# Performance work log

Hardware: AMD Instinct MI355X
Metric: run time of the kernel (lower is better)

Reference implementation:

```python
import jax, jax.numpy as jnp
import numpy as np

B, N, C = 32, 320, 768
H = 12
LT, LS = 64, 256
HD = C // H
MLP_H = 4 * C
EPS = 1e-5


def _ln(x, g, b):
    m = jnp.mean(x, axis=-1, keepdims=True)
    v = jnp.var(x, axis=-1, keepdims=True)
    return (x - m) * jax.lax.rsqrt(v + EPS) * g + b


def setup_inputs() -> dict:
    key = jax.random.key(0)
    ks = jax.random.split(key, 16)
    s = 0.02
    inp = {
        'x': jax.random.normal(ks[0], (B, N, C), jnp.float32),
        'global_index_template': jax.random.randint(ks[1], (B, LT), 0, LT),
        'global_index_search': jax.random.randint(ks[2], (B, LS), 0, LS),
        'g1': jnp.ones((C,), jnp.float32), 'b1': jnp.zeros((C,), jnp.float32),
        'Wqkv': jax.random.normal(ks[3], (C, 3 * C), jnp.float32) * s,
        'Wproj': jax.random.normal(ks[4], (C, C), jnp.float32) * s,
        'bproj': jnp.zeros((C,), jnp.float32),
        'g2': jnp.ones((C,), jnp.float32), 'b2': jnp.zeros((C,), jnp.float32),
        'W1': jax.random.normal(ks[5], (C, MLP_H), jnp.float32) * s,
        'bm1': jnp.zeros((MLP_H,), jnp.float32),
        'W2': jax.random.normal(ks[6], (MLP_H, C), jnp.float32) * s,
        'bm2': jnp.zeros((C,), jnp.float32),
        'Wg': jax.random.normal(ks[7], (C, C), jnp.float32) * s,
        'bg': jnp.zeros((C,), jnp.float32),
        'g3': jnp.ones((C,), jnp.float32), 'b3': jnp.zeros((C,), jnp.float32),
    }
    return inp


def reference(x, global_index_template, global_index_search, g1, b1, Wqkv, Wproj, bproj,
              g2, b2, W1, bm1, W2, bm2, Wg, bg, g3, b3):
    scale = HD ** (-0.5)
    # --- Attention ---
    xn = _ln(x, g1, b1)
    qkv = (xn @ Wqkv).reshape(B, N, 3, H, HD)
    q, k, v = qkv[:, :, 0], qkv[:, :, 1], qkv[:, :, 2]  # [B,N,H,HD]
    logits = jnp.einsum('bnhd,bmhd->bhnm', q, k) * scale
    attn = jax.nn.softmax(logits, axis=-1)  # [B,H,N,N]
    ctx = jnp.einsum('bhnm,bmhd->bnhd', attn, v).reshape(B, N, C)
    x = x + (ctx @ Wproj + bproj)
    # --- MLP ---
    h = jax.nn.gelu(_ln(x, g2, b2) @ W1 + bm1, approximate=False)
    x = x + (h @ W2 + bm2)
    # --- Block-adjacency from attention (avg pooling) ---
    w_ts = jnp.sum(attn[:, :, :LT, LT:], axis=1) / H  # [B,LT,LS]
    w_ts = jax.nn.softmax(w_ts, axis=2)
    adj = jnp.zeros((B, N, N), x.dtype)
    adj = adj.at[:, :LT, LT:].set(w_ts)
    adj = adj.at[:, LT:, :LT].set(jnp.swapaxes(w_ts, 1, 2))
    # --- GCN layer ---
    support = x @ Wg + bg
    x = jnp.einsum('bnm,bmc->bnc', adj, support)
    x = x + _ln(x, g3, b3)
    return x
```

## Files before the change

### kernel.cpp

```cpp
#include <hip/hip_runtime.h>
#include <stdint.h>

#define NB 32
#define NSEQ 320
#define CDIM 768
#define NH 12
#define HD 64
#define MLPH 3072
#define MROWS (NB*NSEQ)

typedef __attribute__((ext_vector_type(8))) short v8s;
typedef __attribute__((ext_vector_type(4))) float v4f;

__device__ __forceinline__ unsigned short f2b(float f){
  unsigned int u = __float_as_uint(f);
  u += 0x7fffu + ((u >> 16) & 1u);
  return (unsigned short)(u >> 16);
}
__device__ __forceinline__ float b2f(unsigned short h){
  return __uint_as_float(((unsigned int)h) << 16);
}
__device__ __forceinline__ void glds16(const unsigned short* g, unsigned short* l){
  __builtin_amdgcn_global_load_lds(
      (const __attribute__((address_space(1))) void*)g,
      (__attribute__((address_space(3))) void*)l, 16, 0, 0);
}

__global__ __launch_bounds__(256)
void castAll(const float* __restrict__ Wqkv, const float* __restrict__ Wproj,
             const float* __restrict__ W1,   const float* __restrict__ W2,
             const float* __restrict__ Wg,
             unsigned short* __restrict__ wqkvT, unsigned short* __restrict__ wprojT,
             unsigned short* __restrict__ w1T,   unsigned short* __restrict__ w2T,
             unsigned short* __restrict__ wgT){
  int bid = blockIdx.x;
  const float* W; unsigned short* Wt; int K, N, KT;
  if (bid < 1728){ W = Wqkv; Wt = wqkvT; K = 768; N = 2304; KT = 24; }
  else if (bid < 1728+576){ bid -= 1728; W = Wproj; Wt = wprojT; K = 768; N = 768; KT = 24; }
  else if (bid < 1728+576+2304){ bid -= 1728+576; W = W1; Wt = w1T; K = 768; N = 3072; KT = 24; }
  else if (bid < 1728+576+2304+2304){ bid -= 1728+576+2304; W = W2; Wt = w2T; K = 3072; N = 768; KT = 96; }
  else { bid -= 1728+576+2304+2304; W = Wg; Wt = wgT; K = 768; N = 768; KT = 24; }
  const int k0 = (bid % KT) * 32, n0 = (bid / KT) * 32;
  __shared__ float tile[32][33];
  const int tx = threadIdx.x & 31, ty = threadIdx.x >> 5;
  #pragma unroll
  for (int i = 0; i < 32; i += 8)
    tile[ty + i][tx] = W[(size_t)(k0 + ty + i) * N + n0 + tx];
  __syncthreads();
  #pragma unroll
  for (int i = 0; i < 32; i += 8)
    Wt[(size_t)(n0 + ty + i) * K + k0 + tx] = f2b(tile[tx][ty + i]);
}

__global__ __launch_bounds__(192)
void ln_to_bf16(const float* __restrict__ x, const float* __restrict__ g,
                const float* __restrict__ be, unsigned short* __restrict__ out){
  const int row = blockIdx.x;
  const int t = threadIdx.x, w = t >> 6, l = t & 63;
  const float4 v = *(const float4*)(x + (size_t)row * CDIM + t * 4);
  float s  = v.x + v.y + v.z + v.w;
  float s2 = v.x*v.x + v.y*v.y + v.z*v.z + v.w*v.w;
  __shared__ float r1[3], r2[3];
  #pragma unroll
  for (int d = 1; d < 64; d <<= 1){ s += __shfl_xor(s, d, 64); s2 += __shfl_xor(s2, d, 64); }
  if (l == 0){ r1[w] = s; r2[w] = s2; }
  __syncthreads();
  const float S = r1[0] + r1[1] + r1[2];
  const float S2 = r2[0] + r2[1] + r2[2];
  const float mean = S * (1.0f / CDIM);
  const float var  = S2 * (1.0f / CDIM) - mean * mean;
  const float rs = rsqrtf(var + 1e-5f);
  const float4 gg = *(const float4*)(g + t * 4);
  const float4 bb = *(const float4*)(be + t * 4);
  ushort4 o;
  o.x = f2b((v.x - mean) * rs * gg.x + bb.x);
  o.y = f2b((v.y - mean) * rs * gg.y + bb.y);
  o.z = f2b((v.z - mean) * rs * gg.z + bb.z);
  o.w = f2b((v.w - mean) * rs * gg.w + bb.w);
  *(ushort4*)(out + (size_t)row * CDIM + t * 4) = o;
}

template<bool BIAS, bool RES, bool GELU, bool WB, bool WF>
__global__ __launch_bounds__(256, 2)
void gemm_bt64(const unsigned short* __restrict__ A, const unsigned short* __restrict__ Bt,
               int N, int K,
               const float* __restrict__ bias, const float* __restrict__ res,
               unsigned short* __restrict__ outb, float* __restrict__ outf){
  __shared__ __align__(16) unsigned short As[128 * 64];
  __shared__ __align__(16) unsigned short Bs[128 * 64];
  const int t = threadIdx.x;
  const int w = t >> 6, l = t & 63;
  const int bm = blockIdx.x, bn = blockIdx.y;
  const int wr = w >> 1, wc = w & 1;
  v4f acc[4][4] = {};

  const int srow = w * 32 + (l >> 3);
  const int scol = ((l & 7) ^ (l >> 3)) * 8;
  const unsigned short* Ag = A + (size_t)(bm * 128 + srow) * K + scol;
  const unsigned short* Bg = Bt + (size_t)(bn * 128 + srow) * K + scol;
  unsigned short* Al = As + (w * 32) * 64;
  unsigned short* Bl = Bs + (w * 32) * 64;

  const int nkt = K >> 6;
  for (int kt = 0; kt < nkt; ++kt){
    const int k0 = kt << 6;
    if (kt) __syncthreads();
    #pragma unroll
    for (int i = 0; i < 4; ++i){
      glds16(Ag + (size_t)(i * 8) * K + k0, Al + i * 8 * 64);
      glds16(Bg + (size_t)(i * 8) * K + k0, Bl + i * 8 * 64);
    }
    __syncthreads();
    #pragma unroll
    for (int ks = 0; ks < 2; ++ks){
      const int kb = ks * 64 + ((l >> 4) << 4);
      v8s af[4], bfr[4];
      #pragma unroll
      for (int mi = 0; mi < 4; ++mi){
        const int r = wr * 64 + mi * 16 + (l & 15);
        af[mi] = *(const v8s*)((const char*)As + r * 128 + (kb ^ ((r & 7) << 4)));
      }
      #pragma unroll
      for (int ni = 0; ni < 4; ++ni){
        const int r = wc * 64 + ni * 16 + (l & 15);
        bfr[ni] = *(const v8s*)((const char*)Bs + r * 128 + (kb ^ ((r & 7) << 4)));
      }
      #pragma unroll
      for (int mi = 0; mi < 4; ++mi)
        #pragma unroll
        for (int ni = 0; ni < 4; ++ni)
          acc[mi][ni] = __builtin_amdgcn_mfma_f32_16x16x32_bf16(af[mi], bfr[ni], acc[mi][ni], 0, 0, 0);
    }
  }

  const int r0 = bm * 128 + wr * 64 + ((l >> 4) << 2);
  const int c0 = bn * 128 + wc * 64 + (l & 15);
  #pragma unroll
  for (int mi = 0; mi < 4; ++mi){
    #pragma unroll
    for (int rr = 0; rr < 4; ++rr){
      const int row = r0 + mi * 16 + rr;
      #pragma unroll
      for (int ni = 0; ni < 4; ++ni){
        const int col = c0 + ni * 16;
        float c = acc[mi][ni][rr];
        if (BIAS) c += bias[col];
        if (RES)  c += res[(size_t)row * N + col];
        if (GELU) c = 0.5f * c * (1.0f + erff(c * 0.70710678118f));
        if (WB) outb[(size_t)row * N + col] = f2b(c);
        if (WF) outf[(size_t)row * N + col] = c;
      }
    }
  }
}

__global__ __launch_bounds__(256, 2)
void attn_kernel(const unsigned short* __restrict__ qkv,
                 unsigned short* __restrict__ ctx,
                 float* __restrict__ wparts){
  __shared__ __align__(16) unsigned short Qs[64 * 72];
  __shared__ __align__(16) unsigned short KV[64 * 72];
  __shared__ __align__(16) unsigned short Ps[64 * 328];
  const int t = threadIdx.x;
  const int w = t >> 6, l = t & 63;
  const int bid = blockIdx.x;
  const int qt = bid % 5;
  const int h  = (bid / 5) % NH;
  const int b  = bid / (5 * NH);
  const size_t base = (size_t)b * NSEQ * 2304 + h * 64;

  {
    const int r = t >> 3, seg = t & 7;
    #pragma unroll
    for (int i = 0; i < 2; ++i){
      const int r2 = r + 32 * i;
      const unsigned short* src = qkv + base + (size_t)(qt * 64 + r2) * 2304 + seg * 8;
      *(uint4*)&Qs[r2 * 72 + seg * 8] = *(const uint4*)src;
    }
  }
  __syncthreads();
  const int qr = 16 * w + (l & 15);
  const v8s aq0 = *(const v8s*)&Qs[qr * 72 + ((l >> 4) << 3)];
  const v8s aq1 = *(const v8s*)&Qs[qr * 72 + 32 + ((l >> 4) << 3)];

  v4f sacc[20] = {};
  for (int kt = 0; kt < 5; ++kt){
    __syncthreads();
    {
      const int r = t >> 3, seg = t & 7;
      #pragma unroll
      for (int i = 0; i < 2; ++i){
        const int r2 = r + 32 * i;
        const unsigned short* src = qkv + base + 768 + (size_t)(kt * 64 + r2) * 2304 + seg * 8;
        *(uint4*)&KV[r2 * 72 + seg * 8] = *(const uint4*)src;
      }
    }
    __syncthreads();
    #pragma unroll
    for (int f = 0; f < 4; ++f){
      const int kr = 16 * f + (l & 15);
      const v8s b0 = *(const v8s*)&KV[kr * 72 + ((l >> 4) << 3)];
      const v8s b1 = *(const v8s*)&KV[kr * 72 + 32 + ((l >> 4) << 3)];
      sacc[kt * 4 + f] = __builtin_amdgcn_mfma_f32_16x16x32_bf16(aq0, b0, sacc[kt * 4 + f], 0, 0, 0);
      sacc[kt * 4 + f] = __builtin_amdgcn_mfma_f32_16x16x32_bf16(aq1, b1, sacc[kt * 4 + f], 0, 0, 0);
    }
  }

  const float scale = 0.125f;
  #pragma unroll
  for (int r = 0; r < 4; ++r){
    float m = -1e30f;
    #pragma unroll
    for (int f = 0; f < 20; ++f) m = fmaxf(m, sacc[f][r]);
    #pragma unroll
    for (int d = 1; d < 16; d <<= 1) m = fmaxf(m, __shfl_xor(m, d, 64));
    const float Ms = m * scale;
    float sum = 0.f;
    #pragma unroll
    for (int f = 0; f < 20; ++f){ float p = expf(sacc[f][r] * scale - Ms); sacc[f][r] = p; sum += p; }
    #pragma unroll
    for (int d = 1; d < 16; d <<= 1) sum += __shfl_xor(sum, d, 64);
    const float inv = 1.0f / sum;
    const int rowq = 16 * w + ((l >> 4) << 2) + r;
    #pragma unroll
    for (int f = 0; f < 20; ++f)
      Ps[rowq * 328 + f * 16 + (l & 15)] = f2b(sacc[f][r] * inv);
    if (qt == 0){
      #pragma unroll
      for (int f = 4; f < 20; ++f)
        wparts[(((size_t)b * NH + h) * 64 + rowq) * 256 + (f - 4) * 16 + (l & 15)] = sacc[f][r] * inv;
    }
  }

  v4f cacc[4] = {};
  for (int kt = 0; kt < 5; ++kt){
    __syncthreads();
    {
      const int m = t & 31, d0 = (t >> 5) * 8;
      #pragma unroll
      for (int i = 0; i < 2; ++i){
        const int m2 = m + 32 * i;
        const unsigned short* src = qkv + base + 1536 + (size_t)(kt * 64 + m2) * 2304 + d0;
        uint4 dv = *(const uint4*)src;
        const unsigned short* e = (const unsigned short*)&dv;
        #pragma unroll
        for (int jj = 0; jj < 8; ++jj) KV[(d0 + jj) * 72 + m2] = e[jj];
      }
    }
    __syncthreads();
    const int pr = 16 * w + (l & 15);
    const v8s pa0 = *(const v8s*)&Ps[pr * 328 + kt * 64 + ((l >> 4) << 3)];
    const v8s pa1 = *(const v8s*)&Ps[pr * 328 + kt * 64 + 32 + ((l >> 4) << 3)];
    #pragma unroll
    for (int f = 0; f < 4; ++f){
      const int vc = 16 * f + (l & 15);
      const v8s bv0 = *(const v8s*)&KV[vc * 72 + ((l >> 4) << 3)];
      const v8s bv1 = *(const v8s*)&KV[vc * 72 + 32 + ((l >> 4) << 3)];
      cacc[f] = __builtin_amdgcn_mfma_f32_16x16x32_bf16(pa0, bv0, cacc[f], 0, 0, 0);
      cacc[f] = __builtin_amdgcn_mfma_f32_16x16x32_bf16(pa1, bv1, cacc[f], 0, 0, 0);
    }
  }
  #pragma unroll
  for (int f = 0; f < 4; ++f)
    #pragma unroll
    for (int rr = 0; rr < 4; ++rr){
      const int rowq = 16 * w + ((l >> 4) << 2) + rr;
      const int col = 16 * f + (l & 15);
      ctx[(size_t)(b * NSEQ + qt * 64 + rowq) * CDIM + h * 64 + col] = f2b(cacc[f][rr]);
    }
}

__global__ __launch_bounds__(256)
void wts_softmax(const float* __restrict__ wparts,
                 unsigned short* __restrict__ wtsb,
                 unsigned short* __restrict__ wtsbT){
  const int row = blockIdx.x;
  const int b = row >> 6, n = row & 63;
  const int j = threadIdx.x;
  const int w = j >> 6, l = j & 63;
  float s = 0.f;
  #pragma unroll
  for (int hh = 0; hh < NH; ++hh)
    s += wparts[(((size_t)b * NH + hh) * 64 + n) * 256 + j];
  s *= (1.0f / NH);
  __shared__ float red[8];
  float m = s;
  #pragma unroll
  for (int d = 1; d < 64; d <<= 1) m = fmaxf(m, __shfl_xor(m, d, 64));
  if (l == 0) red[w] = m;
  __syncthreads();
  m = fmaxf(fmaxf(red[0], red[1]), fmaxf(red[2], red[3]));
  const float e = expf(s - m);
  float sm = e;
  #pragma unroll
  for (int d = 1; d < 64; d <<= 1) sm += __shfl_xor(sm, d, 64);
  if (l == 0) red[4 + w] = sm;
  __syncthreads();
  const float tot = red[4] + red[5] + red[6] + red[7];
  const unsigned short p = f2b(e / tot);
  wtsb [((size_t)b * 64 + n) * 256 + j] = p;
  wtsbT[((size_t)b * 256 + j) * 64 + n] = p;
}

__global__ __launch_bounds__(256)
void transT(const unsigned short* __restrict__ in, unsigned short* __restrict__ out){
  __shared__ unsigned short tile[64][65];
  const int c0 = blockIdx.x * 64, n0 = blockIdx.y * 64, b = blockIdx.z;
  const int tx = threadIdx.x & 31, ty = threadIdx.x >> 5;
  const unsigned short* ib = in + (size_t)b * NSEQ * CDIM;
  unsigned short* ob = out + (size_t)b * CDIM * NSEQ;
  #pragma unroll
  for (int i = 0; i < 64; i += 8){
    const unsigned int v = *(const unsigned int*)&ib[(size_t)(n0 + ty + i) * CDIM + c0 + tx * 2];
    tile[tx * 2][ty + i]     = (unsigned short)(v & 0xffff);
    tile[tx * 2 + 1][ty + i] = (unsigned short)(v >> 16);
  }
  __syncthreads();
  #pragma unroll
  for (int i = 0; i < 64; i += 8){
    const int c = ty + i;
    const unsigned int v = (unsigned int)tile[c][tx * 2] | ((unsigned int)tile[c][tx * 2 + 1] << 16);
    *(unsigned int*)&ob[(size_t)(c0 + c) * NSEQ + n0 + tx * 2] = v;
  }
}

template<int KC, int SH2>
__global__ __launch_bounds__(256, 2)
void graph_gemm(const unsigned short* __restrict__ A, int KTOT,
                const unsigned short* __restrict__ supT, int koff,
                float* __restrict__ y, int rowoff){
  __shared__ __align__(16) unsigned short As[64 * KC];
  __shared__ __align__(16) unsigned short Bs[128 * KC];
  const int t = threadIdx.x, w = t >> 6, l = t & 63;
  const int mt = blockIdx.x, ct = blockIdx.y, b = blockIdx.z;
  const char* Ab = (const char*)(A + (size_t)b * 16384 + (size_t)mt * 64 * KTOT);
  const char* Bb = (const char*)(supT + (size_t)b * CDIM * NSEQ);
  v4f acc[4][2] = {};

  const int nch = KTOT / KC;
  for (int ch = 0; ch < nch; ++ch){
    if (ch) __syncthreads();
    const int kbase = (koff + ch * KC) * 2;
    #pragma unroll
    for (int i = 0; i < KC / 32; ++i){
      const int gi = w * (KC / 32) + i;
      const int X = gi * 1024 + l * 16;
      const int c = X >> SH2;
      const int k2 = (X & (KC * 2 - 1)) ^ ((c & 7) << 4);
      glds16((const unsigned short*)(Ab + (size_t)c * (KTOT * 2) + ch * KC * 2 + k2),
             As + (gi * 512));
    }
    #pragma unroll
    for (int i = 0; i < KC / 16; ++i){
      const int gi = w * (KC / 16) + i;
      const int X = gi * 1024 + l * 16;
      const int c = X >> SH2;
      const int k2 = (X & (KC * 2 - 1)) ^ ((c & 7) << 4);
      glds16((const unsigned short*)(Bb + (size_t)(ct * 128 + c) * (NSEQ * 2) + kbase + k2),
             Bs + (gi * 512));
    }
    __syncthreads();
    #pragma unroll
    for (int ks = 0; ks < KC / 32; ++ks){
      const int kbyte = ks * 64 + ((l >> 4) << 4);
      v8s af[4], bf2[2];
      #pragma unroll
      for (int mi = 0; mi < 4; ++mi){
        const int r = mi * 16 + (l & 15);
        af[mi] = *(const v8s*)((const char*)As + (r << SH2) + (kbyte ^ ((r & 7) << 4)));
      }
      #pragma unroll
      for (int ni = 0; ni < 2; ++ni){
        const int rb = w * 32 + ni * 16 + (l & 15);
        bf2[ni] = *(const v8s*)((const char*)Bs + (rb << SH2) + (kbyte ^ ((rb & 7) << 4)));
      }
      #pragma unroll
      for (int mi = 0; mi < 4; ++mi)
        #pragma unroll
        for (int ni = 0; ni < 2; ++ni)
          acc[mi][ni] = __builtin_amdgcn_mfma_f32_16x16x32_bf16(af[mi], bf2[ni], acc[mi][ni], 0, 0, 0);
    }
  }

  const int r0 = rowoff + mt * 64 + ((l >> 4) << 2);
  const int c0 = ct * 128 + w * 32 + (l & 15);
  #pragma unroll
  for (int mi = 0; mi < 4; ++mi)
    #pragma unroll
    for (int ni = 0; ni < 2; ++ni)
      #pragma unroll
      for (int rr = 0; rr < 4; ++rr)
        y[((size_t)b * NSEQ + r0 + mi * 16 + rr) * CDIM + c0 + ni * 16] = acc[mi][ni][rr];
}

__global__ __launch_bounds__(192)
void ln_final(const float* __restrict__ y, const float* __restrict__ g3,
              const float* __restrict__ b3, float* __restrict__ out){
  const int row = blockIdx.x;
  const int t = threadIdx.x, w = t >> 6, l = t & 63;
  const float4 v = *(const float4*)(y + (size_t)row * CDIM + t * 4);
  float s  = v.x + v.y + v.z + v.w;
  float s2 = v.x*v.x + v.y*v.y + v.z*v.z + v.w*v.w;
  __shared__ float r1[3], r2[3];
  #pragma unroll
  for (int d = 1; d < 64; d <<= 1){ s += __shfl_xor(s, d, 64); s2 += __shfl_xor(s2, d, 64); }
  if (l == 0){ r1[w] = s; r2[w] = s2; }
  __syncthreads();
  const float S = r1[0] + r1[1] + r1[2];
  const float S2 = r2[0] + r2[1] + r2[2];
  const float mean = S * (1.0f / CDIM);
  const float var  = S2 * (1.0f / CDIM) - mean * mean;
  const float rs = rsqrtf(var + 1e-5f);
  const float4 gg = *(const float4*)(g3 + t * 4);
  const float4 bb = *(const float4*)(b3 + t * 4);
  float4 o;
  o.x = v.x + (v.x - mean) * rs * gg.x + bb.x;
  o.y = v.y + (v.y - mean) * rs * gg.y + bb.y;
  o.z = v.z + (v.z - mean) * rs * gg.z + bb.z;
  o.w = v.w + (v.w - mean) * rs * gg.w + bb.w;
  *(float4*)(out + (size_t)row * CDIM + t * 4) = o;
}

extern "C" void kernel_launch(void* const* d_in, const int* in_sizes, int n_in,
                              void* d_out, int out_size, void* d_ws, size_t ws_size,
                              hipStream_t stream){
  (void)in_sizes; (void)n_in; (void)out_size; (void)ws_size;
  const float* x    = (const float*)d_in[0];
  const float* g1   = (const float*)d_in[3];
  const float* b1   = (const float*)d_in[4];
  const float* Wqkv = (const float*)d_in[5];
  const float* Wproj= (const float*)d_in[6];
  const float* bproj= (const float*)d_in[7];
  const float* g2   = (const float*)d_in[8];
  const float* b2   = (const float*)d_in[9];
  const float* W1   = (const float*)d_in[10];
  const float* bm1  = (const float*)d_in[11];
  const float* W2   = (const float*)d_in[12];
  const float* bm2  = (const float*)d_in[13];
  const float* Wg   = (const float*)d_in[14];
  const float* bg   = (const float*)d_in[15];
  const float* g3   = (const float*)d_in[16];
  const float* b3   = (const float*)d_in[17];
  float* out = (float*)d_out;
  char* ws = (char*)d_ws;

  unsigned short* wqkvT = (unsigned short*)(ws + 0);
  unsigned short* wprojT= (unsigned short*)(ws + 3538944);
  unsigned short* w1T   = (unsigned short*)(ws + 4718592);
  unsigned short* w2T   = (unsigned short*)(ws + 9437184);
  unsigned short* wgT   = (unsigned short*)(ws + 14155776);
  unsigned short* xn1   = (unsigned short*)(ws + 15335424);
  unsigned short* qkvb  = (unsigned short*)(ws + 31064064);
  unsigned short* hb    = (unsigned short*)(ws + 15335424);
  unsigned short* supT  = (unsigned short*)(ws + 15335424);
  unsigned short* ctxb  = (unsigned short*)(ws + 78249984);
  unsigned short* x2b   = (unsigned short*)(ws + 78249984);
  unsigned short* xn2   = (unsigned short*)(ws + 93978624);
  unsigned short* supb  = (unsigned short*)(ws + 93978624);
  float*          x1    = (float*)(ws + 109707264);
  float*          wparts= (float*)(ws + 109707264);
  float*          yb    = (float*)(ws + 109707264);
  unsigned short* wtsb  = (unsigned short*)(ws + 141164544);
  unsigned short* wtsbT = (unsigned short*)(ws + 142213120);

  castAll<<<7488, 256, 0, stream>>>(Wqkv, Wproj, W1, W2, Wg,
                                    wqkvT, wprojT, w1T, w2T, wgT);

  ln_to_bf16<<<MROWS, 192, 0, stream>>>(x, g1, b1, xn1);

  gemm_bt64<false,false,false,true,false><<<dim3(80, 18), 256, 0, stream>>>(
      xn1, wqkvT, 2304, CDIM, nullptr, nullptr, qkvb, nullptr);

  attn_kernel<<<NB * NH * 5, 256, 0, stream>>>(qkvb, ctxb, wparts);

  wts_softmax<<<NB * 64, 256, 0, stream>>>(wparts, wtsb, wtsbT);

  gemm_bt64<true,true,false,false,true><<<dim3(80, 6), 256, 0, stream>>>(
      ctxb, wprojT, CDIM, CDIM, bproj, x, nullptr, x1);

  ln_to_bf16<<<MROWS, 192, 0, stream>>>(x1, g2, b2, xn2);

  gemm_bt64<true,false,true,true,false><<<dim3(80, 24), 256, 0, stream>>>(
      xn2, w1T, MLPH, CDIM, bm1, nullptr, hb, nullptr);

  gemm_bt64<true,true,false,true,false><<<dim3(80, 6), 256, 0, stream>>>(
      hb, w2T, CDIM, MLPH, bm2, x1, x2b, nullptr);

  gemm_bt64<true,false,false,true,false><<<dim3(80, 6), 256, 0, stream>>>(
      x2b, wgT, CDIM, CDIM, bg, nullptr, supb, nullptr);

  transT<<<dim3(CDIM/64, NSEQ/64, NB), 256, 0, stream>>>(supb, supT);

  graph_gemm<128, 8><<<dim3(1, 6, NB), 256, 0, stream>>>(wtsb, 256, supT, 64, yb, 0);
  graph_gemm<64, 7><<<dim3(4, 6, NB), 256, 0, stream>>>(wtsbT, 64, supT, 0, yb, 64);

  ln_final<<<MROWS, 192, 0, stream>>>(yb, g3, b3, out);
}
```

Measured before the change: 477.4 us.

## Replace GEMM with triple-buffered, prefetch-ahead pipeline using K-tile 32

Replaces the dense GEMM kernel with a version that keeps three LDS buffers of 32-wide K tiles. Global-to-LDS loads for tile kt+2 are issued while tile kt is being computed, with vmcnt waits and one barrier per step instead of two. It raises the occupancy hint to 3 blocks per CU and raises wave priority around the MFMA block. The aim is to hide global load latency behind the matrix math. The trade-off is that the XOR swizzle on the LDS layout is dropped, which may add LDS bank conflicts, and the 48 KB of LDS per block limits how many blocks fit on a CU.

```diff
diff --git a/kernel.cpp b/kernel.cpp
--- a/kernel.cpp
+++ b/kernel.cpp
@@ -81,56 +81,67 @@
 }
 
 template<bool BIAS, bool RES, bool GELU, bool WB, bool WF>
-__global__ __launch_bounds__(256, 2)
-void gemm_bt64(const unsigned short* __restrict__ A, const unsigned short* __restrict__ Bt,
-               int N, int K,
-               const float* __restrict__ bias, const float* __restrict__ res,
-               unsigned short* __restrict__ outb, float* __restrict__ outf){
-  __shared__ __align__(16) unsigned short As[128 * 64];
-  __shared__ __align__(16) unsigned short Bs[128 * 64];
-  const int t = threadIdx.x;
-  const int w = t >> 6, l = t & 63;
+__global__ __launch_bounds__(256, 3)
+void gemm_cv(const unsigned short* __restrict__ A, const unsigned short* __restrict__ Bt,
+             int N, int K,
+             const float* __restrict__ bias, const float* __restrict__ res,
+             unsigned short* __restrict__ outb, float* __restrict__ outf){
+  __shared__ __align__(16) unsigned short lds[3 * 8192];
+  const int tid = threadIdx.x;
+  const int w = tid >> 6, l = tid & 63;
   const int bm = blockIdx.x, bn = blockIdx.y;
   const int wr = w >> 1, wc = w & 1;
+  const int nkt = K >> 5;
   v4f acc[4][4] = {};
 
-  const int srow = w * 32 + (l >> 3);
-  const int scol = ((l & 7) ^ (l >> 3)) * 8;
+  const int srow = w * 32 + (l >> 2);
+  const int scol = (l & 3) * 8;
   const unsigned short* Ag = A + (size_t)(bm * 128 + srow) * K + scol;
   const unsigned short* Bg = Bt + (size_t)(bn * 128 + srow) * K + scol;
-  unsigned short* Al = As + (w * 32) * 64;
-  unsigned short* Bl = Bs + (w * 32) * 64;
-
-  const int nkt = K >> 6;
-  for (int kt = 0; kt < nkt; ++kt){
-    const int k0 = kt << 6;
-    if (kt) __syncthreads();
-    #pragma unroll
-    for (int i = 0; i < 4; ++i){
-      glds16(Ag + (size_t)(i * 8) * K + k0, Al + i * 8 * 64);
-      glds16(Bg + (size_t)(i * 8) * K + k0, Bl + i * 8 * 64);
-    }
-    __syncthreads();
-    #pragma unroll
-    for (int ks = 0; ks < 2; ++ks){
-      const int kb = ks * 64 + ((l >> 4) << 4);
-      v8s af[4], bfr[4];
-      #pragma unroll
-      for (int mi = 0; mi < 4; ++mi){
-        const int r = wr * 64 + mi * 16 + (l & 15);
-        af[mi] = *(const v8s*)((const char*)As + r * 128 + (kb ^ ((r & 7) << 4)));
-      }
-      #pragma unroll
-      for (int ni = 0; ni < 4; ++ni){
-        const int r = wc * 64 + ni * 16 + (l & 15);
-        bfr[ni] = *(const v8s*)((const char*)Bs + r * 128 + (kb ^ ((r & 7) << 4)));
-      }
-      #pragma unroll
-      for (int mi = 0; mi < 4; ++mi)
-        #pragma unroll
-        for (int ni = 0; ni < 4; ++ni)
-          acc[mi][ni] = __builtin_amdgcn_mfma_f32_16x16x32_bf16(af[mi], bfr[ni], acc[mi][ni], 0, 0, 0);
-    }
+  const int ldst = (w * 32) * 32;
+
+  auto stage = [&](int bufi, int kt){
+    unsigned short* Ab = lds + bufi * 8192;
+    #pragma unroll
+    for (int i = 0; i < 2; ++i){
+      glds16(Ag + (size_t)(i * 16) * K + kt * 32, Ab + ldst + i * 512);
+      glds16(Bg + (size_t)(i * 16) * K + kt * 32, Ab + 4096 + ldst + i * 512);
+    }
+  };
+
+  auto body = [&](int kt, int cbuf){
+    if (kt + 2 < nkt) stage((cbuf + 2) % 3, kt + 2);
+    const unsigned short* Ab = lds + cbuf * 8192;
+    const unsigned short* Bb = Ab + 4096;
+    const int kk = (l >> 4) << 3;
+    v8s af[4], bfr[4];
+    #pragma unroll
+    for (int mi = 0; mi < 4; ++mi)
+      af[mi] = *(const v8s*)&Ab[(wr * 64 + mi * 16 + (l & 15)) * 32 + kk];
+    #pragma unroll
+    for (int ni = 0; ni < 4; ++ni)
+      bfr[ni] = *(const v8s*)&Bb[(wc * 64 + ni * 16 + (l & 15)) * 32 + kk];
+    __builtin_amdgcn_s_setprio(1);
+    #pragma unroll
+    for (int mi = 0; mi < 4; ++mi)
+      #pragma unroll
+      for (int ni = 0; ni < 4; ++ni)
+        acc[mi][ni] = __builtin_amdgcn_mfma_f32_16x16x32_bf16(af[mi], bfr[ni], acc[mi][ni], 0, 0, 0);
+    __builtin_amdgcn_s_setprio(0);
+    if (kt + 2 < nkt)      asm volatile("s_waitcnt vmcnt(4)" ::: "memory");
+    else if (kt + 1 < nkt) asm volatile("s_waitcnt vmcnt(0)" ::: "memory");
+    if (kt + 1 < nkt) __builtin_amdgcn_s_barrier();
+  };
+
+  stage(0, 0); stage(1, 1);
+  asm volatile("s_waitcnt vmcnt(4)" ::: "memory");
+  __builtin_amdgcn_s_barrier();
+
+  #pragma unroll 1
+  for (int base = 0; base < nkt; base += 3){
+    body(base + 0, 0);
+    body(base + 1, 1);
+    body(base + 2, 2);
   }
 
   const int r0 = bm * 128 + wr * 64 + ((l >> 4) << 2);
@@ -468,25 +479,25 @@
 
   ln_to_bf16<<<MROWS, 192, 0, stream>>>(x, g1, b1, xn1);
 
-  gemm_bt64<false,false,false,true,false><<<dim3(80, 18), 256, 0, stream>>>(
+  gemm_cv<false,false,false,true,false><<<dim3(80, 18), 256, 0, stream>>>(
       xn1, wqkvT, 2304, CDIM, nullptr, nullptr, qkvb, nullptr);
 
   attn_kernel<<<NB * NH * 5, 256, 0, stream>>>(qkvb, ctxb, wparts);
 
   wts_softmax<<<NB * 64, 256, 0, stream>>>(wparts, wtsb, wtsbT);
 
-  gemm_bt64<true,true,false,false,true><<<dim3(80, 6), 256, 0, stream>>>(
+  gemm_cv<true,true,false,false,true><<<dim3(80, 6), 256, 0, stream>>>(
       ctxb, wprojT, CDIM, CDIM, bproj, x, nullptr, x1);
 
   ln_to_bf16<<<MROWS, 192, 0, stream>>>(x1, g2, b2, xn2);
 
-  gemm_bt64<true,false,true,true,false><<<dim3(80, 24), 256, 0, stream>>>(
+  gemm_cv<true,false,true,true,false><<<dim3(80, 24), 256, 0, stream>>>(
       xn2, w1T, MLPH, CDIM, bm1, nullptr, hb, nullptr);
 
-  gemm_bt64<true,true,false,true,false><<<dim3(80, 6), 256, 0, stream>>>(
+  gemm_cv<true,true,false,true,false><<<dim3(80, 6), 256, 0, stream>>>(
       hb, w2T, CDIM, MLPH, bm2, x1, x2b, nullptr);
 
-  gemm_bt64<true,false,false,true,false><<<dim3(80, 6), 256, 0, stream>>>(
+  gemm_cv<true,false,false,true,false><<<dim3(80, 6), 256, 0, stream>>>(
       x2b, wgT, CDIM, CDIM, bg, nullptr, supb, nullptr);
 
   transT<<<dim3(CDIM/64, NSEQ/64, NB), 256, 0, stream>>>(supb, supT);
```

Measured after the change: 477.3 us. No clear change (-0.0%).
